# Kernel tuning notes

Hardware: AMD Instinct MI355X
Metric: run time of the kernel (lower is better)

## Reference

```python
import jax, jax.numpy as jnp
import numpy as np

N_STEPS = 4  # fixed-step RK4 stand-in for dopri5 (jit-friendly, same ODE math)

def mlp(params, tt, z):
    # tt: [N,1] time, z: [N,dim] -> velocity [N,dim]
    W1, b1, W2, b2, W3, b3 = params
    h = jnp.tanh(jnp.concatenate([z, tt], axis=-1) @ W1 + b1)
    h = jnp.tanh(h @ W2 + b2)
    return h @ W3 + b3

def f_and_div(params, tt, z):
    # brute-force divergence via dim JVPs (dim=3, exact trace)
    f = lambda zz: mlp(params, tt, zz)
    out = f(z)
    div = jnp.zeros((z.shape[0],), z.dtype)
    for i in range(z.shape[1]):
        tang = jnp.zeros_like(z).at[:, i].set(1.0)
        _, jv = jax.jvp(f, (z,), (tang,))
        div = div + jv[:, i]
    return out, div[:, None]

def dyn(params, s, t0, z):
    # reparametrize per-sample integration t: t0 -> 0 onto s in [0,1]; dt/ds = -t0
    tt = t0 * (1.0 - s)
    f, div = f_and_div(params, tt, z)
    dz = -t0 * f                                   # dz/ds
    ddiv = t0 * div                                # accumulates int_0^{t0} div f dt
    dpen = t0 * jnp.sum(f * f, axis=-1, keepdims=True)  # kinetic-energy OT penalty
    return dz, ddiv, dpen

def integrate_to_t0(params, x, t0):
    h = 1.0 / N_STEPS
    z = x
    d = jnp.zeros((x.shape[0], 1), x.dtype)
    p = jnp.zeros_like(d)
    for k in range(N_STEPS):
        s = k * h
        g = lambda s_, z_: dyn(params, s_, t0, z_)
        k1z, k1d, k1p = g(s, z)
        k2z, k2d, k2p = g(s + 0.5 * h, z + 0.5 * h * k1z)
        k3z, k3d, k3p = g(s + 0.5 * h, z + 0.5 * h * k2z)
        k4z, k4d, k4p = g(s + h, z + h * k3z)
        z = z + (h / 6.0) * (k1z + 2 * k2z + 2 * k3z + k4z)
        d = d + (h / 6.0) * (k1d + 2 * k2d + 2 * k3d + k4d)
        p = p + (h / 6.0) * (k1p + 2 * k2p + 2 * k3p + k4p)
    return z, d, p

def grid_sample_3d_zeros(vol, coords):
    # vol: [D,H,W]; coords: [N,3] in (x,y,z) normalized [-1,1], align_corners=False,
    # padding_mode='zeros' (matches torch grid_sample semantics)
    D, H, W = vol.shape
    px = ((coords[:, 0] + 1.0) * W - 1.0) / 2.0
    py = ((coords[:, 1] + 1.0) * H - 1.0) / 2.0
    pz = ((coords[:, 2] + 1.0) * D - 1.0) / 2.0
    x0 = jnp.floor(px).astype(jnp.int32); y0 = jnp.floor(py).astype(jnp.int32); z0 = jnp.floor(pz).astype(jnp.int32)
    wx1 = px - x0; wy1 = py - y0; wz1 = pz - z0
    out = jnp.zeros(coords.shape[0], vol.dtype)
    for dz_ in (0, 1):
        for dy_ in (0, 1):
            for dx_ in (0, 1):
                ix = x0 + dx_; iy = y0 + dy_; iz = z0 + dz_
                w = (jnp.where(dx_, wx1, 1 - wx1) * jnp.where(dy_, wy1, 1 - wy1)
                     * jnp.where(dz_, wz1, 1 - wz1))
                valid = (ix >= 0) & (ix < W) & (iy >= 0) & (iy < H) & (iz >= 0) & (iz < D)
                v = vol[jnp.clip(iz, 0, D - 1), jnp.clip(iy, 0, H - 1), jnp.clip(ix, 0, W - 1)]
                out = out + jnp.where(valid, v * w, 0.0)
    return out

def setup_inputs() -> dict:
    key = jax.random.key(0)
    ks = jax.random.split(key, 6)
    N, dim, hid, G = 131072, 3, 64, 100
    x = jax.random.normal(ks[0], (N, dim), jnp.float32)
    t = jax.random.uniform(ks[1], (N, 1), jnp.float32)  # in [0,1], some ~0
    W1 = jax.random.normal(ks[2], (dim + 1, hid), jnp.float32) * 0.5
    W2 = jax.random.normal(ks[3], (hid, hid), jnp.float32) * (1.0 / np.sqrt(hid))
    W3 = jax.random.normal(ks[4], (hid, dim), jnp.float32) * (1.0 / np.sqrt(hid))
    base_grid = jax.random.normal(ks[5], (G, G, G, 1), jnp.float32) * 1e-6
    return {"x": x, "t": t, "W1": W1, "b1": jnp.zeros((hid,), jnp.float32),
            "W2": W2, "b2": jnp.zeros((hid,), jnp.float32),
            "W3": W3, "b3": jnp.zeros((dim,), jnp.float32), "base_grid": base_grid}

def reference(x, t, W1, b1, W2, b2, W3, b3, base_grid):
    params = (W1, b1, W2, b2, W3, b3)
    z_end, d_end, _pen = integrate_to_t0(params, x, t)
    mask = (t > 0)  # [N,1]
    z_t0 = jnp.where(mask, z_end, x)
    div_acc = jnp.where(mask, d_end, 0.0)
    vol = base_grid[..., 0]  # [D,H,W] after torch permute(3,0,1,2)
    logp = grid_sample_3d_zeros(vol, z_t0 / 5.0) - div_acc[:, 0]
    return logp
```

## Files before the change

### kernel.cpp

```cpp
#include <hip/hip_runtime.h>
#include <math.h>

#define NSAMP 131072

typedef _Float16 half8v __attribute__((ext_vector_type(8)));
typedef float    f32x4  __attribute__((ext_vector_type(4)));

__device__ __forceinline__ float fast_tanh(float x) {
    float e = __builtin_amdgcn_exp2f(x * 2.885390081777927f);
    return fmaf(-2.0f, __builtin_amdgcn_rcpf(e + 1.0f), 1.0f);
}

__global__ __launch_bounds__(256, 2)
void cnf_logp_kernel(const float* __restrict__ xin, const float* __restrict__ tin,
                     const float* __restrict__ W1, const float* __restrict__ b1,
                     const float* __restrict__ W2, const float* __restrict__ b2,
                     const float* __restrict__ W3, const float* __restrict__ b3,
                     const float* __restrict__ vol, float* __restrict__ out)
{
    const int tid  = threadIdx.x;
    const int lane = tid & 63;
    const int col  = lane & 15;
    const int g    = lane >> 4;


    half8v A1[4];
    #pragma unroll
    for (int kq = 0; kq < 4; ++kq) {
        half8v a;
        #pragma unroll
        for (int e = 0; e < 8; ++e) a[e] = (_Float16)0.0f;
        const int krow = kq*16 + col;
        #pragma unroll
        for (int e = 0; e < 4; ++e) {
            const float w = W1[e*64 + krow];
            const _Float16 whi = (_Float16)w;
            const _Float16 wlo = (_Float16)(w - (float)whi);
            _Float16 v = (_Float16)0.0f;
            if (g == 0 || g == 2)      v = whi;
            else if (g == 1)           v = wlo;
            else {
                const float bv = b1[krow];
                const _Float16 bhi = (_Float16)bv;
                if (e == 0)      v = bhi;
                else if (e == 1) v = (_Float16)(bv - (float)bhi);
            }
            a[e] = v;
        }
        A1[kq] = a;
    }

    half8v AW2[8];
    half8v AHW[8];
    #pragma unroll
    for (int nt = 0; nt < 4; ++nt) {
        const int j = nt*16 + col;
        const float w3j0 = W3[j*3+0], w3j1 = W3[j*3+1], w3j2 = W3[j*3+2];
        #pragma unroll
        for (int kh = 0; kh < 2; ++kh) {
            #pragma unroll
            for (int e = 0; e < 8; ++e) {
                const int k = kh*32 + 4*g + (e & 3) + 16*(e >> 2);
                const float w2v = W2[k*64 + j];
                const float gv  = W1[0*64+k]*w3j0 + W1[1*64+k]*w3j1 + W1[2*64+k]*w3j2;
                AW2[nt*2 + kh][e] = (_Float16)w2v;
                AHW[nt*2 + kh][e] = (_Float16)(w2v * gv);
            }
        }
    }
    f32x4 b2v[4];
    #pragma unroll
    for (int nt = 0; nt < 4; ++nt) {
        #pragma unroll
        for (int r = 0; r < 4; ++r) b2v[nt][r] = b2[nt*16 + 4*g + r];
    }
    half8v A3[2];
    #pragma unroll
    for (int kp = 0; kp < 2; ++kp) {
        #pragma unroll
        for (int e = 0; e < 8; ++e) {
            const int j = kp*32 + 4*g + (e & 3) + 16*(e >> 2);
            A3[kp][e] = (col < 3) ? (_Float16)W3[j*3 + col] : (_Float16)0.0f;
        }
    }
    const float b3c0 = b3[0], b3c1 = b3[1], b3c2 = b3[2];

    const int idx = blockIdx.x*64 + (tid >> 6)*16 + col;
    const float x0v = xin[idx*3 + 0], x1v = xin[idx*3 + 1], x2v = xin[idx*3 + 2];
    const float t0  = tin[idx];

    float z0 = x0v, z1 = x1v, z2 = x2v;
    float dacc = 0.0f;
    const float hstep = 0.25f;
    float kz0 = 0.f, kz1 = 0.f, kz2 = 0.f;
    float sa0 = 0.f, sa1 = 0.f, sa2 = 0.f;

    const bool g2f = (g == 2), g3f = (g == 3);

    #pragma unroll 1
    for (int it = 0; it < 16; ++it) {
        const int st   = it & 3;
        const int step = it >> 2;
        const float alpha = (st == 0) ? 0.0f : ((st == 3) ? hstep : 0.5f * hstep);
        const float wgt   = (st == 1 || st == 2) ? (hstep * (1.0f/3.0f)) : (hstep * (1.0f/6.0f));
        const float s     = (float)step * hstep + alpha;
        const float zi0 = fmaf(alpha, kz0, z0);
        const float zi1 = fmaf(alpha, kz1, z1);
        const float zi2 = fmaf(alpha, kz2, z2);
        const float tt  = t0 * (1.0f - s);

        const _Float16 z0h = (_Float16)zi0, z1h = (_Float16)zi1,
                       z2h = (_Float16)zi2, tth = (_Float16)tt;
        const _Float16 z0l = (_Float16)(zi0 - (float)z0h);
        const _Float16 z1l = (_Float16)(zi1 - (float)z1h);
        const _Float16 z2l = (_Float16)(zi2 - (float)z2h);
        const _Float16 ttl = (_Float16)(tt  - (float)tth);
        half8v B1;
        #pragma unroll
        for (int e = 0; e < 8; ++e) B1[e] = (_Float16)0.0f;
        B1[0] = g3f ? (_Float16)1.0f : (g2f ? z0l : z0h);
        B1[1] = g3f ? (_Float16)1.0f : (g2f ? z1l : z1h);
        B1[2] = g3f ? (_Float16)0.0f : (g2f ? z2l : z2h);
        B1[3] = g3f ? (_Float16)0.0f : (g2f ? ttl : tth);

        float h[4][4];
        #pragma unroll
        for (int kq = 0; kq < 4; ++kq) {
            f32x4 z4; z4[0]=0.f; z4[1]=0.f; z4[2]=0.f; z4[3]=0.f;
            z4 = __builtin_amdgcn_mfma_f32_16x16x32_f16(A1[kq], B1, z4, 0, 0, 0);
            #pragma unroll
            for (int r = 0; r < 4; ++r) h[kq][r] = fast_tanh(z4[r]);
        }

        half8v BH[2], BQ[2];
        half8v hone;
        #pragma unroll
        for (int e = 0; e < 8; ++e) hone[e] = (_Float16)1.0f;
        #pragma unroll
        for (int kh = 0; kh < 2; ++kh) {
            #pragma unroll
            for (int e = 0; e < 8; ++e)
                BH[kh][e] = (_Float16)h[kh*2 + (e >> 2)][e & 3];
            BQ[kh] = hone - BH[kh]*BH[kh];
        }

        f32x4 a2[4], d2[4];
        #pragma unroll
        for (int nt = 0; nt < 4; ++nt) {
            f32x4 acc = b2v[nt];
            acc = __builtin_amdgcn_mfma_f32_16x16x32_f16(AW2[nt*2+0], BH[0], acc, 0, 0, 0);
            acc = __builtin_amdgcn_mfma_f32_16x16x32_f16(AW2[nt*2+1], BH[1], acc, 0, 0, 0);
            a2[nt] = acc;
            f32x4 z4; z4[0]=0.f; z4[1]=0.f; z4[2]=0.f; z4[3]=0.f;
            z4  = __builtin_amdgcn_mfma_f32_16x16x32_f16(AHW[nt*2+0], BQ[0], z4, 0, 0, 0);
            z4  = __builtin_amdgcn_mfma_f32_16x16x32_f16(AHW[nt*2+1], BQ[1], z4, 0, 0, 0);
            d2[nt] = z4;
        }

        float h2v[4][4];
        float pdv = 0.0f;
        #pragma unroll
        for (int nt = 0; nt < 4; ++nt) {
            #pragma unroll
            for (int r = 0; r < 4; ++r) {
                const float h2 = fast_tanh(a2[nt][r]);
                h2v[nt][r] = h2;
                const float s2 = fmaf(-h2, h2, 1.0f);
                pdv = fmaf(s2, d2[nt][r], pdv);
            }
        }
        half8v B2h[2];
        #pragma unroll
        for (int kp = 0; kp < 2; ++kp) {
            #pragma unroll
            for (int e = 0; e < 8; ++e)
                B2h[kp][e] = (_Float16)h2v[kp*2 + (e >> 2)][e & 3];
        }
        f32x4 fD; fD[0]=0.f; fD[1]=0.f; fD[2]=0.f; fD[3]=0.f;
        fD = __builtin_amdgcn_mfma_f32_16x16x32_f16(A3[0], B2h[0], fD, 0, 0, 0);
        fD = __builtin_amdgcn_mfma_f32_16x16x32_f16(A3[1], B2h[1], fD, 0, 0, 0);

        pdv += __shfl_xor(pdv, 16);
        pdv += __shfl_xor(pdv, 32);
        const float f0 = __shfl(fD[0], col) + b3c0;
        const float f1 = __shfl(fD[1], col) + b3c1;
        const float f2 = __shfl(fD[2], col) + b3c2;

        const float v0 = -t0 * f0, v1 = -t0 * f1, v2 = -t0 * f2;
        const float vd =  t0 * pdv;
        kz0 = v0; kz1 = v1; kz2 = v2;
        dacc = fmaf(wgt, vd, dacc);
        if (st == 0) { sa0 = wgt*v0; sa1 = wgt*v1; sa2 = wgt*v2; }
        else         { sa0 = fmaf(wgt, v0, sa0); sa1 = fmaf(wgt, v1, sa1); sa2 = fmaf(wgt, v2, sa2); }
        if (st == 3) { z0 += sa0; z1 += sa1; z2 += sa2; }
    }

    if (g == 0) {
        const bool m = (t0 > 0.0f);
        const float q0 = m ? z0 : x0v;
        const float q1 = m ? z1 : x1v;
        const float q2 = m ? z2 : x2v;
        const float dfin = m ? dacc : 0.0f;

        const float px = ((q0 * 0.2f + 1.0f) * 100.0f - 1.0f) * 0.5f;
        const float py = ((q1 * 0.2f + 1.0f) * 100.0f - 1.0f) * 0.5f;
        const float pz = ((q2 * 0.2f + 1.0f) * 100.0f - 1.0f) * 0.5f;
        const float fx = floorf(px), fy = floorf(py), fz = floorf(pz);
        const int ix0 = (int)fx, iy0 = (int)fy, iz0 = (int)fz;
        const float wx1 = px - fx, wy1 = py - fy, wz1 = pz - fz;

        float gs = 0.0f;
        #pragma unroll
        for (int c = 0; c < 8; ++c) {
            const int dxc = c & 1, dyc = (c >> 1) & 1, dzc = (c >> 2) & 1;
            const int ix = ix0 + dxc, iy = iy0 + dyc, iz = iz0 + dzc;
            const float w = (dxc ? wx1 : 1.0f - wx1)
                          * (dyc ? wy1 : 1.0f - wy1)
                          * (dzc ? wz1 : 1.0f - wz1);
            if (ix >= 0 && ix < 100 && iy >= 0 && iy < 100 && iz >= 0 && iz < 100)
                gs += vol[(iz * 100 + iy) * 100 + ix] * w;
        }
        out[idx] = gs - dfin;
    }
}

extern "C" void kernel_launch(void* const* d_in, const int* in_sizes, int n_in,
                              void* d_out, int out_size, void* d_ws, size_t ws_size,
                              hipStream_t stream) {
    const float* x    = (const float*)d_in[0];
    const float* t    = (const float*)d_in[1];
    const float* W1   = (const float*)d_in[2];
    const float* b1   = (const float*)d_in[3];
    const float* W2   = (const float*)d_in[4];
    const float* b2   = (const float*)d_in[5];
    const float* W3   = (const float*)d_in[6];
    const float* b3   = (const float*)d_in[7];
    const float* vol  = (const float*)d_in[8];
    float* out = (float*)d_out;

    dim3 grid(NSAMP / 64), block(256);
    cnf_logp_kernel<<<grid, block, 0, stream>>>(x, t, W1, b1, W2, b2, W3, b3, vol, out);
}
```

Before: 110.3 us.

## Process two sample tiles per wave for ILP and pack fp16 with cvt_pkrtz

Each wave now integrates two independent 16-sample tiles at once, interleaving their MFMA and tanh chains to hide MFMA latency and amortize the weight fragments held in registers. The grid is halved and launch bounds drop to one block per SIMD minimum to allow more registers. The fp32-to-fp16 conversions of hidden activations use packed round-toward-zero conversions instead of per-element casts, which slightly changes rounding. The cost is higher register pressure, possibly lower occupancy, and fewer blocks to fill the GPU.

Measured after the change: 136.6 us. 1.24x slower.

```diff
diff --git a/kernel.cpp b/kernel.cpp
--- a/kernel.cpp
+++ b/kernel.cpp
@@ -4,14 +4,29 @@
 #define NSAMP 131072
 
 typedef _Float16 half8v __attribute__((ext_vector_type(8)));
+typedef __fp16   fp16x2 __attribute__((ext_vector_type(2)));
+typedef __fp16   fp16x4 __attribute__((ext_vector_type(4)));
+typedef __fp16   fp16x8 __attribute__((ext_vector_type(8)));
 typedef float    f32x4  __attribute__((ext_vector_type(4)));
+typedef float    f32x8  __attribute__((ext_vector_type(8)));
 
 __device__ __forceinline__ float fast_tanh(float x) {
     float e = __builtin_amdgcn_exp2f(x * 2.885390081777927f);
     return fmaf(-2.0f, __builtin_amdgcn_rcpf(e + 1.0f), 1.0f);
 }
 
-__global__ __launch_bounds__(256, 2)
+__device__ __forceinline__ half8v pack8rtz(f32x8 v) {
+    fp16x2 p0 = __builtin_amdgcn_cvt_pkrtz(v[0], v[1]);
+    fp16x2 p1 = __builtin_amdgcn_cvt_pkrtz(v[2], v[3]);
+    fp16x2 p2 = __builtin_amdgcn_cvt_pkrtz(v[4], v[5]);
+    fp16x2 p3 = __builtin_amdgcn_cvt_pkrtz(v[6], v[7]);
+    fp16x4 q0 = __builtin_shufflevector(p0, p1, 0, 1, 2, 3);
+    fp16x4 q1 = __builtin_shufflevector(p2, p3, 0, 1, 2, 3);
+    fp16x8 r  = __builtin_shufflevector(q0, q1, 0, 1, 2, 3, 4, 5, 6, 7);
+    return __builtin_bit_cast(half8v, r);
+}
+
+__global__ __launch_bounds__(256, 1)
 void cnf_logp_kernel(const float* __restrict__ xin, const float* __restrict__ tin,
                      const float* __restrict__ W1, const float* __restrict__ b1,
                      const float* __restrict__ W2, const float* __restrict__ b2,
@@ -85,16 +100,23 @@
     }
     const float b3c0 = b3[0], b3c1 = b3[1], b3c2 = b3[2];
 
-    const int idx = blockIdx.x*64 + (tid >> 6)*16 + col;
-    const float x0v = xin[idx*3 + 0], x1v = xin[idx*3 + 1], x2v = xin[idx*3 + 2];
-    const float t0  = tin[idx];
-
-    float z0 = x0v, z1 = x1v, z2 = x2v;
-    float dacc = 0.0f;
+    const int idxA = blockIdx.x*128 + (tid >> 6)*16 + col;
+    const int idxB = idxA + 64;
+
+    float x0v[2], x1v[2], x2v[2], t0[2];
+    x0v[0] = xin[idxA*3 + 0]; x1v[0] = xin[idxA*3 + 1]; x2v[0] = xin[idxA*3 + 2];
+    x0v[1] = xin[idxB*3 + 0]; x1v[1] = xin[idxB*3 + 1]; x2v[1] = xin[idxB*3 + 2];
+    t0[0] = tin[idxA]; t0[1] = tin[idxB];
+
+    float z0[2], z1[2], z2[2], dacc[2];
+    float kz0[2], kz1[2], kz2[2], sa0[2], sa1[2], sa2[2];
+    #pragma unroll
+    for (int ss = 0; ss < 2; ++ss) {
+        z0[ss] = x0v[ss]; z1[ss] = x1v[ss]; z2[ss] = x2v[ss];
+        dacc[ss] = 0.f; kz0[ss] = 0.f; kz1[ss] = 0.f; kz2[ss] = 0.f;
+        sa0[ss] = 0.f; sa1[ss] = 0.f; sa2[ss] = 0.f;
+    }
     const float hstep = 0.25f;
-    float kz0 = 0.f, kz1 = 0.f, kz2 = 0.f;
-    float sa0 = 0.f, sa1 = 0.f, sa2 = 0.f;
-
     const bool g2f = (g == 2), g3f = (g == 3);
 
     #pragma unroll 1
@@ -104,123 +126,152 @@
         const float alpha = (st == 0) ? 0.0f : ((st == 3) ? hstep : 0.5f * hstep);
         const float wgt   = (st == 1 || st == 2) ? (hstep * (1.0f/3.0f)) : (hstep * (1.0f/6.0f));
         const float s     = (float)step * hstep + alpha;
-        const float zi0 = fmaf(alpha, kz0, z0);
-        const float zi1 = fmaf(alpha, kz1, z1);
-        const float zi2 = fmaf(alpha, kz2, z2);
-        const float tt  = t0 * (1.0f - s);
-
-        const _Float16 z0h = (_Float16)zi0, z1h = (_Float16)zi1,
-                       z2h = (_Float16)zi2, tth = (_Float16)tt;
-        const _Float16 z0l = (_Float16)(zi0 - (float)z0h);
-        const _Float16 z1l = (_Float16)(zi1 - (float)z1h);
-        const _Float16 z2l = (_Float16)(zi2 - (float)z2h);
-        const _Float16 ttl = (_Float16)(tt  - (float)tth);
-        half8v B1;
-        #pragma unroll
-        for (int e = 0; e < 8; ++e) B1[e] = (_Float16)0.0f;
-        B1[0] = g3f ? (_Float16)1.0f : (g2f ? z0l : z0h);
-        B1[1] = g3f ? (_Float16)1.0f : (g2f ? z1l : z1h);
-        B1[2] = g3f ? (_Float16)0.0f : (g2f ? z2l : z2h);
-        B1[3] = g3f ? (_Float16)0.0f : (g2f ? ttl : tth);
-
-        float h[4][4];
-        #pragma unroll
-        for (int kq = 0; kq < 4; ++kq) {
-            f32x4 z4; z4[0]=0.f; z4[1]=0.f; z4[2]=0.f; z4[3]=0.f;
-            z4 = __builtin_amdgcn_mfma_f32_16x16x32_f16(A1[kq], B1, z4, 0, 0, 0);
-            #pragma unroll
-            for (int r = 0; r < 4; ++r) h[kq][r] = fast_tanh(z4[r]);
-        }
-
-        half8v BH[2], BQ[2];
+        const float oms   = 1.0f - s;
+
+        half8v B1[2];
+        #pragma unroll
+        for (int ss = 0; ss < 2; ++ss) {
+            const float zi0 = fmaf(alpha, kz0[ss], z0[ss]);
+            const float zi1 = fmaf(alpha, kz1[ss], z1[ss]);
+            const float zi2 = fmaf(alpha, kz2[ss], z2[ss]);
+            const float tt  = t0[ss] * oms;
+            const _Float16 z0h = (_Float16)zi0, z1h = (_Float16)zi1,
+                           z2h = (_Float16)zi2, tth = (_Float16)tt;
+            const _Float16 z0l = (_Float16)(zi0 - (float)z0h);
+            const _Float16 z1l = (_Float16)(zi1 - (float)z1h);
+            const _Float16 z2l = (_Float16)(zi2 - (float)z2h);
+            const _Float16 ttl = (_Float16)(tt  - (float)tth);
+            half8v B;
+            #pragma unroll
+            for (int e = 0; e < 8; ++e) B[e] = (_Float16)0.0f;
+            B[0] = g3f ? (_Float16)1.0f : (g2f ? z0l : z0h);
+            B[1] = g3f ? (_Float16)1.0f : (g2f ? z1l : z1h);
+            B[2] = g3f ? (_Float16)0.0f : (g2f ? z2l : z2h);
+            B[3] = g3f ? (_Float16)0.0f : (g2f ? ttl : tth);
+            B1[ss] = B;
+        }
+
+        f32x8 hv[2][2];
+        #pragma unroll
+        for (int ss = 0; ss < 2; ++ss) {
+            #pragma unroll
+            for (int kq = 0; kq < 4; ++kq) {
+                f32x4 z4; z4[0]=0.f; z4[1]=0.f; z4[2]=0.f; z4[3]=0.f;
+                z4 = __builtin_amdgcn_mfma_f32_16x16x32_f16(A1[kq], B1[ss], z4, 0, 0, 0);
+                #pragma unroll
+                for (int r = 0; r < 4; ++r)
+                    hv[ss][kq >> 1][(kq & 1)*4 + r] = fast_tanh(z4[r]);
+            }
+        }
+
+        half8v BH[2][2], BQ[2][2];
         half8v hone;
         #pragma unroll
         for (int e = 0; e < 8; ++e) hone[e] = (_Float16)1.0f;
         #pragma unroll
-        for (int kh = 0; kh < 2; ++kh) {
-            #pragma unroll
-            for (int e = 0; e < 8; ++e)
-                BH[kh][e] = (_Float16)h[kh*2 + (e >> 2)][e & 3];
-            BQ[kh] = hone - BH[kh]*BH[kh];
-        }
-
-        f32x4 a2[4], d2[4];
-        #pragma unroll
-        for (int nt = 0; nt < 4; ++nt) {
-            f32x4 acc = b2v[nt];
-            acc = __builtin_amdgcn_mfma_f32_16x16x32_f16(AW2[nt*2+0], BH[0], acc, 0, 0, 0);
-            acc = __builtin_amdgcn_mfma_f32_16x16x32_f16(AW2[nt*2+1], BH[1], acc, 0, 0, 0);
-            a2[nt] = acc;
-            f32x4 z4; z4[0]=0.f; z4[1]=0.f; z4[2]=0.f; z4[3]=0.f;
-            z4  = __builtin_amdgcn_mfma_f32_16x16x32_f16(AHW[nt*2+0], BQ[0], z4, 0, 0, 0);
-            z4  = __builtin_amdgcn_mfma_f32_16x16x32_f16(AHW[nt*2+1], BQ[1], z4, 0, 0, 0);
-            d2[nt] = z4;
-        }
-
-        float h2v[4][4];
-        float pdv = 0.0f;
-        #pragma unroll
-        for (int nt = 0; nt < 4; ++nt) {
-            #pragma unroll
-            for (int r = 0; r < 4; ++r) {
-                const float h2 = fast_tanh(a2[nt][r]);
-                h2v[nt][r] = h2;
-                const float s2 = fmaf(-h2, h2, 1.0f);
-                pdv = fmaf(s2, d2[nt][r], pdv);
-            }
-        }
-        half8v B2h[2];
-        #pragma unroll
-        for (int kp = 0; kp < 2; ++kp) {
-            #pragma unroll
-            for (int e = 0; e < 8; ++e)
-                B2h[kp][e] = (_Float16)h2v[kp*2 + (e >> 2)][e & 3];
-        }
-        f32x4 fD; fD[0]=0.f; fD[1]=0.f; fD[2]=0.f; fD[3]=0.f;
-        fD = __builtin_amdgcn_mfma_f32_16x16x32_f16(A3[0], B2h[0], fD, 0, 0, 0);
-        fD = __builtin_amdgcn_mfma_f32_16x16x32_f16(A3[1], B2h[1], fD, 0, 0, 0);
-
-        pdv += __shfl_xor(pdv, 16);
-        pdv += __shfl_xor(pdv, 32);
-        const float f0 = __shfl(fD[0], col) + b3c0;
-        const float f1 = __shfl(fD[1], col) + b3c1;
-        const float f2 = __shfl(fD[2], col) + b3c2;
-
-        const float v0 = -t0 * f0, v1 = -t0 * f1, v2 = -t0 * f2;
-        const float vd =  t0 * pdv;
-        kz0 = v0; kz1 = v1; kz2 = v2;
-        dacc = fmaf(wgt, vd, dacc);
-        if (st == 0) { sa0 = wgt*v0; sa1 = wgt*v1; sa2 = wgt*v2; }
-        else         { sa0 = fmaf(wgt, v0, sa0); sa1 = fmaf(wgt, v1, sa1); sa2 = fmaf(wgt, v2, sa2); }
-        if (st == 3) { z0 += sa0; z1 += sa1; z2 += sa2; }
+        for (int ss = 0; ss < 2; ++ss) {
+            #pragma unroll
+            for (int kh = 0; kh < 2; ++kh) {
+                BH[ss][kh] = pack8rtz(hv[ss][kh]);
+                BQ[ss][kh] = hone - BH[ss][kh]*BH[ss][kh];
+            }
+        }
+
+        f32x4 a2[2][4], d2[2][4];
+        #pragma unroll
+        for (int ss = 0; ss < 2; ++ss) {
+            #pragma unroll
+            for (int nt = 0; nt < 4; ++nt) {
+                f32x4 acc = b2v[nt];
+                acc = __builtin_amdgcn_mfma_f32_16x16x32_f16(AW2[nt*2+0], BH[ss][0], acc, 0, 0, 0);
+                acc = __builtin_amdgcn_mfma_f32_16x16x32_f16(AW2[nt*2+1], BH[ss][1], acc, 0, 0, 0);
+                a2[ss][nt] = acc;
+                f32x4 z4; z4[0]=0.f; z4[1]=0.f; z4[2]=0.f; z4[3]=0.f;
+                z4  = __builtin_amdgcn_mfma_f32_16x16x32_f16(AHW[nt*2+0], BQ[ss][0], z4, 0, 0, 0);
+                z4  = __builtin_amdgcn_mfma_f32_16x16x32_f16(AHW[nt*2+1], BQ[ss][1], z4, 0, 0, 0);
+                d2[ss][nt] = z4;
+            }
+        }
+
+        float pdv[2];
+        f32x8 h2v[2][2];
+        #pragma unroll
+        for (int ss = 0; ss < 2; ++ss) {
+            pdv[ss] = 0.0f;
+            #pragma unroll
+            for (int nt = 0; nt < 4; ++nt) {
+                #pragma unroll
+                for (int r = 0; r < 4; ++r) {
+                    const float h2 = fast_tanh(a2[ss][nt][r]);
+                    h2v[ss][nt >> 1][(nt & 1)*4 + r] = h2;
+                    const float s2 = fmaf(-h2, h2, 1.0f);
+                    pdv[ss] = fmaf(s2, d2[ss][nt][r], pdv[ss]);
+                }
+            }
+        }
+        f32x4 fD[2];
+        #pragma unroll
+        for (int ss = 0; ss < 2; ++ss) {
+            half8v B2h0 = pack8rtz(h2v[ss][0]);
+            half8v B2h1 = pack8rtz(h2v[ss][1]);
+            f32x4 f4; f4[0]=0.f; f4[1]=0.f; f4[2]=0.f; f4[3]=0.f;
+            f4 = __builtin_amdgcn_mfma_f32_16x16x32_f16(A3[0], B2h0, f4, 0, 0, 0);
+            f4 = __builtin_amdgcn_mfma_f32_16x16x32_f16(A3[1], B2h1, f4, 0, 0, 0);
+            fD[ss] = f4;
+        }
+
+        #pragma unroll
+        for (int ss = 0; ss < 2; ++ss) {
+            float pd = pdv[ss];
+            pd += __shfl_xor(pd, 16);
+            pd += __shfl_xor(pd, 32);
+            const float f0 = __shfl(fD[ss][0], col) + b3c0;
+            const float f1 = __shfl(fD[ss][1], col) + b3c1;
+            const float f2 = __shfl(fD[ss][2], col) + b3c2;
+
+            const float v0 = -t0[ss] * f0, v1 = -t0[ss] * f1, v2 = -t0[ss] * f2;
+            const float vd =  t0[ss] * pd;
+            kz0[ss] = v0; kz1[ss] = v1; kz2[ss] = v2;
+            dacc[ss] = fmaf(wgt, vd, dacc[ss]);
+            if (st == 0) { sa0[ss] = wgt*v0; sa1[ss] = wgt*v1; sa2[ss] = wgt*v2; }
+            else {
+                sa0[ss] = fmaf(wgt, v0, sa0[ss]);
+                sa1[ss] = fmaf(wgt, v1, sa1[ss]);
+                sa2[ss] = fmaf(wgt, v2, sa2[ss]);
+            }
+            if (st == 3) { z0[ss] += sa0[ss]; z1[ss] += sa1[ss]; z2[ss] += sa2[ss]; }
+        }
     }
 
     if (g == 0) {
-        const bool m = (t0 > 0.0f);
-        const float q0 = m ? z0 : x0v;
-        const float q1 = m ? z1 : x1v;
-        const float q2 = m ? z2 : x2v;
-        const float dfin = m ? dacc : 0.0f;
-
-        const float px = ((q0 * 0.2f + 1.0f) * 100.0f - 1.0f) * 0.5f;
-        const float py = ((q1 * 0.2f + 1.0f) * 100.0f - 1.0f) * 0.5f;
-        const float pz = ((q2 * 0.2f + 1.0f) * 100.0f - 1.0f) * 0.5f;
-        const float fx = floorf(px), fy = floorf(py), fz = floorf(pz);
-        const int ix0 = (int)fx, iy0 = (int)fy, iz0 = (int)fz;
-        const float wx1 = px - fx, wy1 = py - fy, wz1 = pz - fz;
-
-        float gs = 0.0f;
-        #pragma unroll
-        for (int c = 0; c < 8; ++c) {
-            const int dxc = c & 1, dyc = (c >> 1) & 1, dzc = (c >> 2) & 1;
-            const int ix = ix0 + dxc, iy = iy0 + dyc, iz = iz0 + dzc;
-            const float w = (dxc ? wx1 : 1.0f - wx1)
-                          * (dyc ? wy1 : 1.0f - wy1)
-                          * (dzc ? wz1 : 1.0f - wz1);
-            if (ix >= 0 && ix < 100 && iy >= 0 && iy < 100 && iz >= 0 && iz < 100)
-                gs += vol[(iz * 100 + iy) * 100 + ix] * w;
-        }
-        out[idx] = gs - dfin;
+        #pragma unroll
+        for (int ss = 0; ss < 2; ++ss) {
+            const bool m = (t0[ss] > 0.0f);
+            const float q0 = m ? z0[ss] : x0v[ss];
+            const float q1 = m ? z1[ss] : x1v[ss];
+            const float q2 = m ? z2[ss] : x2v[ss];
+            const float dfin = m ? dacc[ss] : 0.0f;
+
+            const float px = ((q0 * 0.2f + 1.0f) * 100.0f - 1.0f) * 0.5f;
+            const float py = ((q1 * 0.2f + 1.0f) * 100.0f - 1.0f) * 0.5f;
+            const float pz = ((q2 * 0.2f + 1.0f) * 100.0f - 1.0f) * 0.5f;
+            const float fx = floorf(px), fy = floorf(py), fz = floorf(pz);
+            const int ix0 = (int)fx, iy0 = (int)fy, iz0 = (int)fz;
+            const float wx1 = px - fx, wy1 = py - fy, wz1 = pz - fz;
+
+            float gs = 0.0f;
+            #pragma unroll
+            for (int c = 0; c < 8; ++c) {
+                const int dxc = c & 1, dyc = (c >> 1) & 1, dzc = (c >> 2) & 1;
+                const int ix = ix0 + dxc, iy = iy0 + dyc, iz = iz0 + dzc;
+                const float w = (dxc ? wx1 : 1.0f - wx1)
+                              * (dyc ? wy1 : 1.0f - wy1)
+                              * (dzc ? wz1 : 1.0f - wz1);
+                if (ix >= 0 && ix < 100 && iy >= 0 && iy < 100 && iz >= 0 && iz < 100)
+                    gs += vol[(iz * 100 + iy) * 100 + ix] * w;
+            }
+            out[ss ? idxB : idxA] = gs - dfin;
+        }
     }
 }
 
@@ -238,6 +289,6 @@
     const float* vol  = (const float*)d_in[8];
     float* out = (float*)d_out;
 
-    dim3 grid(NSAMP / 64), block(256);
+    dim3 grid(NSAMP / 128), block(256);
     cnf_logp_kernel<<<grid, block, 0, stream>>>(x, t, W1, b1, W2, b2, W3, b3, vol, out);
 }
```
